# Optimization experiments

Measured on AMD Instinct MI355X. Metric: run time of the kernel, lower is better.

## Reference

```python
import jax, jax.numpy as jnp
import numpy as np

B, BANDS, N, IN_C, F, C = 4096, 5, 30, 512, 128, 9

def setup_inputs() -> dict:
    key = jax.random.key(0)
    ks = jax.random.split(key, 10)
    def glorot(k, shape):
        lim = float(np.sqrt(6.0 / (shape[0] + shape[-1])))
        return jax.random.uniform(k, shape, jnp.float32, -lim, lim)
    return {
        "real": jax.random.normal(ks[0], (B, N, IN_C), jnp.float32),
        "imag": jax.random.normal(ks[1], (B, N, IN_C), jnp.float32),
        "graph": jax.random.normal(ks[2], (B, BANDS, N, N), jnp.float32),
        "W1": glorot(ks[3], (IN_C, F)),
        "b1": jnp.zeros((F,), jnp.float32),
        "W2": glorot(ks[4], (F, F)),
        "b2": jnp.zeros((F,), jnp.float32),
        "Wlin": glorot(ks[5], (F, 1)),
        "blin": jnp.zeros((1,), jnp.float32),
        "Wconv": glorot(ks[6], (C, N)),  # Conv1d(30, C, k=1) weight squeezed
        "bconv": jnp.zeros((C,), jnp.float32),
    }

def _norm_adj(graph):
    # adj = mean over bands; PyG from_scipy_sparse_matrix keeps only the
    # nonzero PATTERN (edge weights are discarded in the original code).
    adj = jnp.mean(graph, axis=1)                       # [B, N, N]
    A = (adj != 0).astype(jnp.float32)
    eye = jnp.eye(A.shape[-1], dtype=jnp.float32)
    A_hat = jnp.where(eye > 0, 1.0, A)                  # add remaining self-loops
    deg = A_hat.sum(-1)                                 # [B, N]
    dinv = jnp.where(deg > 0, jax.lax.rsqrt(deg), 0.0)
    return dinv[..., :, None] * A_hat * dinv[..., None, :]  # D^-1/2 (A+I) D^-1/2

def reference(real, imag, graph, W1, b1, W2, b2, Wlin, blin, Wconv, bconv):
    An = _norm_adj(graph)                               # [B, N, N]
    # GCNConv layer 1: propagate(x @ W) + bias, then ReLU (dropout = eval identity)
    h = jnp.einsum('bnm,bmf->bnf', An, real @ W1) + b1
    h = jax.nn.relu(h)
    # GCNConv layer 2
    h = jnp.einsum('bnm,bmf->bnf', An, h @ W2) + b2
    h = jax.nn.relu(h)
    # lin: [B, N, F] -> [B, N], relu, then Conv1d(30->C, k=1) over length-1 axis
    x = jax.nn.relu((h @ Wlin + blin).squeeze(-1))      # [B, N]
    out = x @ Wconv.T + bconv                           # [B, C]
    return out
```

## Files before the change

### kernel.cpp

```cpp
#include <hip/hip_runtime.h>
#include <cstdint>

#define B_SZ 4096
#define NN   30
#define INC  512
#define FF   128
#define CC   9

typedef short short8 __attribute__((ext_vector_type(8)));
typedef float f32x4 __attribute__((ext_vector_type(4)));
typedef unsigned short us4 __attribute__((ext_vector_type(4)));

__device__ inline void split_bf16(float x, unsigned short& hi, unsigned short& lo) {
  uint32_t bits = __float_as_uint(x);
  hi = (unsigned short)(bits >> 16);
  float hif = __uint_as_float(((uint32_t)hi) << 16);
  float r = x - hif;
  lo = (unsigned short)(__float_as_uint(r) >> 16);
}

__global__ __launch_bounds__(128) void k_norm_adj(const float* __restrict__ graph,
                                                  float* __restrict__ An) {
  __shared__ float Ah[NN * NN];
  __shared__ float dinv[NN];
  const int b = blockIdx.x;
  const float* g = graph + (long)b * 5 * NN * NN;
  for (int e = threadIdx.x; e < NN * NN; e += 128) {
    float s = g[e] + g[e + 900] + g[e + 1800] + g[e + 2700] + g[e + 3600];
    float mean = s * 0.2f;
    int i = e / NN;
    int j = e - i * NN;
    Ah[e] = (mean != 0.0f || i == j) ? 1.0f : 0.0f;
  }
  __syncthreads();
  if (threadIdx.x < NN) {
    float d = 0.f;
#pragma unroll
    for (int j = 0; j < NN; ++j) d += Ah[threadIdx.x * NN + j];
    dinv[threadIdx.x] = (d > 0.f) ? (1.0f / sqrtf(d)) : 0.0f;
  }
  __syncthreads();
  float* ob = An + (long)b * NN * NN;
  for (int e = threadIdx.x; e < NN * NN; e += 128) {
    int i = e / NN;
    int j = e - i * NN;
    ob[e] = Ah[e] * dinv[i] * dinv[j];
  }
}

__global__ __launch_bounds__(256) void k_prep_w(const float* __restrict__ W,
                                                unsigned short* __restrict__ Wth,
                                                unsigned short* __restrict__ Wtl,
                                                int K) {
  int idx = blockIdx.x * 256 + threadIdx.x;
  if (idx >= K * FF) return;
  int k = idx >> 7;
  int n = idx & 127;
  unsigned short h, l;
  split_bf16(W[idx], h, l);
  Wth[n * K + k] = h;
  Wtl[n * K + k] = l;
}

#define LDT 40
#define LDY 132

__global__ __launch_bounds__(256, 2) void k_fused(
    const float* __restrict__ real,
    const float* __restrict__ An,
    const unsigned short* __restrict__ W1h, const unsigned short* __restrict__ W1l,
    const unsigned short* __restrict__ W2h, const unsigned short* __restrict__ W2l,
    const float* __restrict__ b1v, const float* __restrict__ b2v,
    const float* __restrict__ Wlin, const float* __restrict__ blin,
    const float* __restrict__ Wconv, const float* __restrict__ bconv,
    float* __restrict__ out) {
  __shared__ __align__(16) char smem[65168];
  unsigned short* H1h = (unsigned short*)smem;
  unsigned short* H1l = (unsigned short*)(smem + 16384);
  unsigned short* Ash = (unsigned short*)(smem + 32768);
  unsigned short* Asl = (unsigned short*)(smem + 32768 + 64 * LDT * 2);
  float* Ylds = (float*)(smem + 32768);
  float* partial = (float*)(smem + 64448);
  float* xs = (float*)(smem + 64928);

  const int tid = threadIdx.x;
  const int wave = tid >> 6;
  const int lane = tid & 63;
  const int fr = lane & 15;
  const int fq = lane >> 4;
  const int wc = wave;
  const long b0 = (long)blockIdx.x * 2;

  f32x4 acc[4][2];
#pragma unroll
  for (int i = 0; i < 4; ++i)
#pragma unroll
    for (int j = 0; j < 2; ++j) acc[i][j] = (f32x4){0.f, 0.f, 0.f, 0.f};

  const int r0 = tid >> 3, kq0 = tid & 7;
  const int r1 = r0 + 32;
  int i0 = r0 & 31; if (i0 >= NN) i0 -= NN;
  int i1 = r1 & 31; if (i1 >= NN) i1 -= NN;
  const float* aptr0 = real + ((b0 + (r0 >> 5)) * NN + i0) * (long)INC + kq0 * 4;
  const float* aptr1 = real + ((b0 + (r1 >> 5)) * NN + i1) * (long)INC + kq0 * 4;

  float4 pA0 = *(const float4*)(aptr0);
  float4 pA1 = *(const float4*)(aptr1);

  for (int k0 = 0; k0 < INC; k0 += 32) {
    __syncthreads();
    {
      us4 h, l;
      split_bf16(pA0.x, ((unsigned short*)&h)[0], ((unsigned short*)&l)[0]);
      split_bf16(pA0.y, ((unsigned short*)&h)[1], ((unsigned short*)&l)[1]);
      split_bf16(pA0.z, ((unsigned short*)&h)[2], ((unsigned short*)&l)[2]);
      split_bf16(pA0.w, ((unsigned short*)&h)[3], ((unsigned short*)&l)[3]);
      *(us4*)(Ash + r0 * LDT + kq0 * 4) = h;
      *(us4*)(Asl + r0 * LDT + kq0 * 4) = l;
      split_bf16(pA1.x, ((unsigned short*)&h)[0], ((unsigned short*)&l)[0]);
      split_bf16(pA1.y, ((unsigned short*)&h)[1], ((unsigned short*)&l)[1]);
      split_bf16(pA1.z, ((unsigned short*)&h)[2], ((unsigned short*)&l)[2]);
      split_bf16(pA1.w, ((unsigned short*)&h)[3], ((unsigned short*)&l)[3]);
      *(us4*)(Ash + r1 * LDT + kq0 * 4) = h;
      *(us4*)(Asl + r1 * LDT + kq0 * 4) = l;
    }
    if (k0 + 32 < INC) {
      pA0 = *(const float4*)(aptr0 + k0 + 32);
      pA1 = *(const float4*)(aptr1 + k0 + 32);
    }
    __syncthreads();
    short8 bh[2], bl2[2];
#pragma unroll
    for (int ct = 0; ct < 2; ++ct) {
      const long n = wc * 32 + ct * 16 + fr;
      bh[ct]  = *(const short8*)(W1h + n * INC + k0 + fq * 8);
      bl2[ct] = *(const short8*)(W1l + n * INC + k0 + fq * 8);
    }
#pragma unroll
    for (int rt = 0; rt < 4; ++rt) {
      const int m = rt * 16 + fr;
      short8 ah = *(const short8*)(Ash + m * LDT + fq * 8);
      short8 al = *(const short8*)(Asl + m * LDT + fq * 8);
#pragma unroll
      for (int ct = 0; ct < 2; ++ct) {
        acc[rt][ct] = __builtin_amdgcn_mfma_f32_16x16x32_bf16(ah, bh[ct], acc[rt][ct], 0, 0, 0);
        acc[rt][ct] = __builtin_amdgcn_mfma_f32_16x16x32_bf16(al, bh[ct], acc[rt][ct], 0, 0, 0);
        acc[rt][ct] = __builtin_amdgcn_mfma_f32_16x16x32_bf16(ah, bl2[ct], acc[rt][ct], 0, 0, 0);
      }
    }
  }
  __syncthreads();

#pragma unroll
  for (int rt = 0; rt < 4; ++rt) {
#pragma unroll
    for (int r = 0; r < 4; ++r) {
      const int row = rt * 16 + fq * 4 + r;
      const int ii = row & 31;
      if (ii < NN) {
        const int yrow = (row >> 5) * NN + ii;
#pragma unroll
        for (int ct = 0; ct < 2; ++ct)
          Ylds[yrow * LDY + wc * 32 + ct * 16 + fr] = acc[rt][ct][r];
      }
    }
  }
  {
    const int pr = wave;
    const int prow = (pr >> 1) * 32 + 30 + (pr & 1);
    *(uint32_t*)(H1h + prow * 128 + lane * 2) = 0u;
    *(uint32_t*)(H1l + prow * 128 + lane * 2) = 0u;
  }
  __syncthreads();

  const int f = tid & 127;
  const int bu = __builtin_amdgcn_readfirstlane(tid >> 7);
  const float* Arow = An + (b0 + bu) * (NN * NN);
  {
    float y[NN];
#pragma unroll
    for (int m = 0; m < NN; ++m) y[m] = Ylds[(bu * NN + m) * LDY + f];
    const float bias1 = b1v[f];
#pragma unroll 1
    for (int i = 0; i < NN; ++i) {
      float h = bias1;
#pragma unroll
      for (int m = 0; m < NN; ++m) h = fmaf(Arow[i * NN + m], y[m], h);
      h = fmaxf(h, 0.f);
      unsigned short hh, hl;
      split_bf16(h, hh, hl);
      const int row = bu * 32 + i;
      const int idx = row * 128 + ((((f >> 3) ^ (row & 7)) << 3) | (f & 7));
      H1h[idx] = hh;
      H1l[idx] = hl;
    }
  }
  __syncthreads();

  f32x4 acc2[4][2];
#pragma unroll
  for (int i = 0; i < 4; ++i)
#pragma unroll
    for (int j = 0; j < 2; ++j) acc2[i][j] = (f32x4){0.f, 0.f, 0.f, 0.f};

#pragma unroll
  for (int ks = 0; ks < 4; ++ks) {
    short8 bh[2], bl2[2];
#pragma unroll
    for (int ct = 0; ct < 2; ++ct) {
      const long n = wc * 32 + ct * 16 + fr;
      bh[ct]  = *(const short8*)(W2h + n * FF + ks * 32 + fq * 8);
      bl2[ct] = *(const short8*)(W2l + n * FF + ks * 32 + fq * 8);
    }
#pragma unroll
    for (int rt = 0; rt < 4; ++rt) {
      const int row = rt * 16 + fr;
      const int gs = (((ks * 4 + fq) ^ (row & 7)) << 3);
      short8 ah = *(const short8*)(H1h + row * 128 + gs);
      short8 al = *(const short8*)(H1l + row * 128 + gs);
#pragma unroll
      for (int ct = 0; ct < 2; ++ct) {
        acc2[rt][ct] = __builtin_amdgcn_mfma_f32_16x16x32_bf16(ah, bh[ct], acc2[rt][ct], 0, 0, 0);
        acc2[rt][ct] = __builtin_amdgcn_mfma_f32_16x16x32_bf16(al, bh[ct], acc2[rt][ct], 0, 0, 0);
        acc2[rt][ct] = __builtin_amdgcn_mfma_f32_16x16x32_bf16(ah, bl2[ct], acc2[rt][ct], 0, 0, 0);
      }
    }
  }
#pragma unroll
  for (int rt = 0; rt < 4; ++rt) {
#pragma unroll
    for (int r = 0; r < 4; ++r) {
      const int row = rt * 16 + fq * 4 + r;
      const int ii = row & 31;
      if (ii < NN) {
        const int yrow = (row >> 5) * NN + ii;
#pragma unroll
        for (int ct = 0; ct < 2; ++ct)
          Ylds[yrow * LDY + wc * 32 + ct * 16 + fr] = acc2[rt][ct][r];
      }
    }
  }
  __syncthreads();

  {
    float t[NN];
#pragma unroll
    for (int m = 0; m < NN; ++m) t[m] = Ylds[(bu * NN + m) * LDY + f];
    const float bias2 = b2v[f];
    const float wl = Wlin[f];
#pragma unroll 1
    for (int i = 0; i < NN; ++i) {
      float h = bias2;
#pragma unroll
      for (int m = 0; m < NN; ++m) h = fmaf(Arow[i * NN + m], t[m], h);
      float c = fmaxf(h, 0.f) * wl;
#pragma unroll
      for (int off = 32; off > 0; off >>= 1) c += __shfl_down(c, off, 64);
      if (lane == 0) partial[wave * NN + i] = c;
    }
  }
  __syncthreads();
  if (tid < 2 * NN) {
    const int bb = tid / NN, i = tid - bb * NN;
    float x = partial[bb * 2 * NN + i] + partial[(bb * 2 + 1) * NN + i] + blin[0];
    xs[bb * NN + i] = fmaxf(x, 0.f);
  }
  __syncthreads();
  if (tid < 2 * CC) {
    const int bb = tid / CC, c = tid - bb * CC;
    float o = bconv[c];
#pragma unroll
    for (int i = 0; i < NN; ++i) o = fmaf(xs[bb * NN + i], Wconv[c * NN + i], o);
    out[(b0 + bb) * CC + c] = o;
  }
}

extern "C" void kernel_launch(void* const* d_in, const int* in_sizes, int n_in,
                              void* d_out, int out_size, void* d_ws, size_t ws_size,
                              hipStream_t stream) {
  const float* real  = (const float*)d_in[0];
  const float* graph = (const float*)d_in[2];
  const float* W1    = (const float*)d_in[3];
  const float* b1    = (const float*)d_in[4];
  const float* W2    = (const float*)d_in[5];
  const float* b2    = (const float*)d_in[6];
  const float* Wlin  = (const float*)d_in[7];
  const float* blin  = (const float*)d_in[8];
  const float* Wconv = (const float*)d_in[9];
  const float* bconv = (const float*)d_in[10];
  float* out = (float*)d_out;

  float* An = (float*)d_ws;
  unsigned short* W1h = (unsigned short*)(An + (long)B_SZ * NN * NN);
  unsigned short* W1l = W1h + INC * FF;
  unsigned short* W2h = W1l + INC * FF;
  unsigned short* W2l = W2h + FF * FF;

  k_norm_adj<<<B_SZ, 128, 0, stream>>>(graph, An);
  k_prep_w<<<(INC * FF + 255) / 256, 256, 0, stream>>>(W1, W1h, W1l, INC);
  k_prep_w<<<(FF * FF + 255) / 256, 256, 0, stream>>>(W2, W2h, W2l, FF);
  k_fused<<<B_SZ / 2, 256, 0, stream>>>(real, An, W1h, W1l, W2h, W2l,
                                        b1, b2, Wlin, blin, Wconv, bconv, out);
}
```

Before: 651.7 us.

## Fuse adjacency normalization into main kernel, one batch per block, double-buffer staging

```diff
diff --git a/kernel.cpp b/kernel.cpp
--- a/kernel.cpp
+++ b/kernel.cpp
@@ -19,33 +19,33 @@
   lo = (unsigned short)(__float_as_uint(r) >> 16);
 }
 
-__global__ __launch_bounds__(128) void k_norm_adj(const float* __restrict__ graph,
-                                                  float* __restrict__ An) {
-  __shared__ float Ah[NN * NN];
-  __shared__ float dinv[NN];
-  const int b = blockIdx.x;
-  const float* g = graph + (long)b * 5 * NN * NN;
-  for (int e = threadIdx.x; e < NN * NN; e += 128) {
-    float s = g[e] + g[e + 900] + g[e + 1800] + g[e + 2700] + g[e + 3600];
-    float mean = s * 0.2f;
-    int i = e / NN;
-    int j = e - i * NN;
-    Ah[e] = (mean != 0.0f || i == j) ? 1.0f : 0.0f;
-  }
-  __syncthreads();
-  if (threadIdx.x < NN) {
-    float d = 0.f;
-#pragma unroll
-    for (int j = 0; j < NN; ++j) d += Ah[threadIdx.x * NN + j];
-    dinv[threadIdx.x] = (d > 0.f) ? (1.0f / sqrtf(d)) : 0.0f;
-  }
-  __syncthreads();
-  float* ob = An + (long)b * NN * NN;
-  for (int e = threadIdx.x; e < NN * NN; e += 128) {
-    int i = e / NN;
-    int j = e - i * NN;
-    ob[e] = Ah[e] * dinv[i] * dinv[j];
-  }
+__device__ inline void split4(const float4 v, us4& h, us4& l) {
+  unsigned short* hp = (unsigned short*)&h;
+  unsigned short* lp = (unsigned short*)&l;
+  split_bf16(v.x, hp[0], lp[0]);
+  split_bf16(v.y, hp[1], lp[1]);
+  split_bf16(v.z, hp[2], lp[2]);
+  split_bf16(v.w, hp[3], lp[3]);
+}
+
+__device__ inline void split8(const float4 v0, const float4 v1, short8& h, short8& l) {
+  unsigned short* hp = (unsigned short*)&h;
+  unsigned short* lp = (unsigned short*)&l;
+  split_bf16(v0.x, hp[0], lp[0]);
+  split_bf16(v0.y, hp[1], lp[1]);
+  split_bf16(v0.z, hp[2], lp[2]);
+  split_bf16(v0.w, hp[3], lp[3]);
+  split_bf16(v1.x, hp[4], lp[4]);
+  split_bf16(v1.y, hp[5], lp[5]);
+  split_bf16(v1.z, hp[6], lp[6]);
+  split_bf16(v1.w, hp[7], lp[7]);
+}
+
+__device__ inline void wg_barrier() {
+  __builtin_amdgcn_sched_barrier(0);
+  asm volatile("s_waitcnt lgkmcnt(0)" ::: "memory");
+  __builtin_amdgcn_s_barrier();
+  __builtin_amdgcn_sched_barrier(0);
 }
 
 __global__ __launch_bounds__(256) void k_prep_w(const float* __restrict__ W,
@@ -64,214 +64,282 @@
 
 #define LDT 40
 #define LDY 132
-
-__global__ __launch_bounds__(256, 2) void k_fused(
+#define ANW 32
+
+__global__ __launch_bounds__(256, 4) void k_fused(
     const float* __restrict__ real,
-    const float* __restrict__ An,
+    const float* __restrict__ graph,
     const unsigned short* __restrict__ W1h, const unsigned short* __restrict__ W1l,
     const unsigned short* __restrict__ W2h, const unsigned short* __restrict__ W2l,
     const float* __restrict__ b1v, const float* __restrict__ b2v,
     const float* __restrict__ Wlin, const float* __restrict__ blin,
     const float* __restrict__ Wconv, const float* __restrict__ bconv,
     float* __restrict__ out) {
-  __shared__ __align__(16) char smem[65168];
-  unsigned short* H1h = (unsigned short*)smem;
-  unsigned short* H1l = (unsigned short*)(smem + 16384);
-  unsigned short* Ash = (unsigned short*)(smem + 32768);
-  unsigned short* Asl = (unsigned short*)(smem + 32768 + 64 * LDT * 2);
-  float* Ylds = (float*)(smem + 32768);
-  float* partial = (float*)(smem + 64448);
-  float* xs = (float*)(smem + 64928);
+  __shared__ __align__(16) float AnL[NN * ANW];
+  __shared__ float dinvL[NN + 2];
+  __shared__ __align__(16) char stageY[15840];
+  __shared__ __align__(16) float H1[32 * LDY];
+  __shared__ float partial[2][NN];
+  __shared__ float xs[NN];
+
+  unsigned short* Sh = (unsigned short*)stageY;
+  unsigned short* Sl = (unsigned short*)(stageY + 2 * 32 * LDT * 2);
+  float* Ylds = (float*)stageY;
 
   const int tid = threadIdx.x;
   const int wave = tid >> 6;
   const int lane = tid & 63;
   const int fr = lane & 15;
   const int fq = lane >> 4;
-  const int wc = wave;
-  const long b0 = (long)blockIdx.x * 2;
-
-  f32x4 acc[4][2];
-#pragma unroll
-  for (int i = 0; i < 4; ++i)
+  const int wc = wave * 32;
+  const long b = blockIdx.x;
+
+  float4 g0, g1, g2, g3, g4;
+  const int e4 = tid * 4;
+  const bool gact = (e4 < NN * NN);
+  {
+    const float* gp = graph + b * 5 * NN * NN + (gact ? e4 : 0);
+    g0 = *(const float4*)(gp);
+    g1 = *(const float4*)(gp + 900);
+    g2 = *(const float4*)(gp + 1800);
+    g3 = *(const float4*)(gp + 2700);
+    g4 = *(const float4*)(gp + 3600);
+  }
+
+  const int arow = tid >> 3;
+  const int akq = tid & 7;
+  const int ar = arow < NN ? arow : NN - 1;
+  const float* abase = real + (b * NN + ar) * (long)INC + akq * 4;
+  float4 pa[2];
+  pa[0] = *(const float4*)(abase);
+  pa[1] = *(const float4*)(abase + 32);
+
+  const unsigned short* w1hp = W1h + (long)(wc + fr) * INC + fq * 8;
+  const unsigned short* w1lp = W1l + (long)(wc + fr) * INC + fq * 8;
+  short8 bh0 = *(const short8*)(w1hp);
+  short8 bh1 = *(const short8*)(w1hp + 16 * INC);
+  short8 bl0 = *(const short8*)(w1lp);
+  short8 bl1 = *(const short8*)(w1lp + 16 * INC);
+
+  if (gact) {
+    float mm0 = g0.x + g1.x + g2.x + g3.x + g4.x;
+    float mm1 = g0.y + g1.y + g2.y + g3.y + g4.y;
+    float mm2 = g0.z + g1.z + g2.z + g3.z + g4.z;
+    float mm3 = g0.w + g1.w + g2.w + g3.w + g4.w;
+    float mm[4] = {mm0, mm1, mm2, mm3};
+#pragma unroll
+    for (int q = 0; q < 4; ++q) {
+      int e = e4 + q;
+      int i = e / NN, j = e - i * NN;
+      AnL[i * ANW + j] = (mm[q] * 0.2f != 0.0f || i == j) ? 1.0f : 0.0f;
+    }
+  }
+  if (tid < NN) { AnL[tid * ANW + 30] = 0.f; AnL[tid * ANW + 31] = 0.f; }
+  wg_barrier();
+  if (tid < NN) {
+    float d = 0.f;
+    const float4* r4 = (const float4*)(AnL + tid * ANW);
+#pragma unroll
+    for (int q = 0; q < 8; ++q) { float4 v = r4[q]; d += v.x + v.y + v.z + v.w; }
+    dinvL[tid] = (d > 0.f) ? (1.0f / sqrtf(d)) : 0.f;
+  }
+  wg_barrier();
+  if (gact) {
+#pragma unroll
+    for (int q = 0; q < 4; ++q) {
+      int e = e4 + q;
+      int i = e / NN, j = e - i * NN;
+      AnL[i * ANW + j] *= dinvL[i] * dinvL[j];
+    }
+  }
+
+  {
+    us4 h, l;
+    split4(pa[0], h, l);
+    *(us4*)(Sh + arow * LDT + akq * 4) = h;
+    *(us4*)(Sl + arow * LDT + akq * 4) = l;
+  }
+  pa[0] = *(const float4*)(abase + 64);
+  wg_barrier();
+
+  f32x4 acc[2][2];
+#pragma unroll
+  for (int i = 0; i < 2; ++i)
 #pragma unroll
     for (int j = 0; j < 2; ++j) acc[i][j] = (f32x4){0.f, 0.f, 0.f, 0.f};
 
-  const int r0 = tid >> 3, kq0 = tid & 7;
-  const int r1 = r0 + 32;
-  int i0 = r0 & 31; if (i0 >= NN) i0 -= NN;
-  int i1 = r1 & 31; if (i1 >= NN) i1 -= NN;
-  const float* aptr0 = real + ((b0 + (r0 >> 5)) * NN + i0) * (long)INC + kq0 * 4;
-  const float* aptr1 = real + ((b0 + (r1 >> 5)) * NN + i1) * (long)INC + kq0 * 4;
-
-  float4 pA0 = *(const float4*)(aptr0);
-  float4 pA1 = *(const float4*)(aptr1);
-
-  for (int k0 = 0; k0 < INC; k0 += 32) {
-    __syncthreads();
-    {
+#pragma unroll
+  for (int t = 0; t < 16; ++t) {
+    const int cur = t & 1;
+    const int nxt = cur ^ 1;
+    short8 ah0 = *(const short8*)(Sh + cur * 32 * LDT + fr * LDT + fq * 8);
+    short8 ah1 = *(const short8*)(Sh + cur * 32 * LDT + (16 + fr) * LDT + fq * 8);
+    short8 al0 = *(const short8*)(Sl + cur * 32 * LDT + fr * LDT + fq * 8);
+    short8 al1 = *(const short8*)(Sl + cur * 32 * LDT + (16 + fr) * LDT + fq * 8);
+
+    short8 nbh0, nbh1, nbl0, nbl1;
+    if (t + 1 < 16) {
       us4 h, l;
-      split_bf16(pA0.x, ((unsigned short*)&h)[0], ((unsigned short*)&l)[0]);
-      split_bf16(pA0.y, ((unsigned short*)&h)[1], ((unsigned short*)&l)[1]);
-      split_bf16(pA0.z, ((unsigned short*)&h)[2], ((unsigned short*)&l)[2]);
-      split_bf16(pA0.w, ((unsigned short*)&h)[3], ((unsigned short*)&l)[3]);
-      *(us4*)(Ash + r0 * LDT + kq0 * 4) = h;
-      *(us4*)(Asl + r0 * LDT + kq0 * 4) = l;
-      split_bf16(pA1.x, ((unsigned short*)&h)[0], ((unsigned short*)&l)[0]);
-      split_bf16(pA1.y, ((unsigned short*)&h)[1], ((unsigned short*)&l)[1]);
-      split_bf16(pA1.z, ((unsigned short*)&h)[2], ((unsigned short*)&l)[2]);
-      split_bf16(pA1.w, ((unsigned short*)&h)[3], ((unsigned short*)&l)[3]);
-      *(us4*)(Ash + r1 * LDT + kq0 * 4) = h;
-      *(us4*)(Asl + r1 * LDT + kq0 * 4) = l;
-    }
-    if (k0 + 32 < INC) {
-      pA0 = *(const float4*)(aptr0 + k0 + 32);
-      pA1 = *(const float4*)(aptr1 + k0 + 32);
-    }
-    __syncthreads();
-    short8 bh[2], bl2[2];
-#pragma unroll
-    for (int ct = 0; ct < 2; ++ct) {
-      const long n = wc * 32 + ct * 16 + fr;
-      bh[ct]  = *(const short8*)(W1h + n * INC + k0 + fq * 8);
-      bl2[ct] = *(const short8*)(W1l + n * INC + k0 + fq * 8);
-    }
-#pragma unroll
-    for (int rt = 0; rt < 4; ++rt) {
-      const int m = rt * 16 + fr;
-      short8 ah = *(const short8*)(Ash + m * LDT + fq * 8);
-      short8 al = *(const short8*)(Asl + m * LDT + fq * 8);
-#pragma unroll
-      for (int ct = 0; ct < 2; ++ct) {
-        acc[rt][ct] = __builtin_amdgcn_mfma_f32_16x16x32_bf16(ah, bh[ct], acc[rt][ct], 0, 0, 0);
-        acc[rt][ct] = __builtin_amdgcn_mfma_f32_16x16x32_bf16(al, bh[ct], acc[rt][ct], 0, 0, 0);
-        acc[rt][ct] = __builtin_amdgcn_mfma_f32_16x16x32_bf16(ah, bl2[ct], acc[rt][ct], 0, 0, 0);
-      }
-    }
-  }
-  __syncthreads();
-
-#pragma unroll
-  for (int rt = 0; rt < 4; ++rt) {
+      split4(pa[(t + 1) & 1], h, l);
+      *(us4*)(Sh + nxt * 32 * LDT + arow * LDT + akq * 4) = h;
+      *(us4*)(Sl + nxt * 32 * LDT + arow * LDT + akq * 4) = l;
+      if (t + 3 < 16) pa[(t + 1) & 1] = *(const float4*)(abase + (t + 3) * 32);
+      nbh0 = *(const short8*)(w1hp + (t + 1) * 32);
+      nbh1 = *(const short8*)(w1hp + 16 * INC + (t + 1) * 32);
+      nbl0 = *(const short8*)(w1lp + (t + 1) * 32);
+      nbl1 = *(const short8*)(w1lp + 16 * INC + (t + 1) * 32);
+    }
+
+    acc[0][0] = __builtin_amdgcn_mfma_f32_16x16x32_bf16(ah0, bh0, acc[0][0], 0, 0, 0);
+    acc[0][0] = __builtin_amdgcn_mfma_f32_16x16x32_bf16(al0, bh0, acc[0][0], 0, 0, 0);
+    acc[0][0] = __builtin_amdgcn_mfma_f32_16x16x32_bf16(ah0, bl0, acc[0][0], 0, 0, 0);
+    acc[0][1] = __builtin_amdgcn_mfma_f32_16x16x32_bf16(ah0, bh1, acc[0][1], 0, 0, 0);
+    acc[0][1] = __builtin_amdgcn_mfma_f32_16x16x32_bf16(al0, bh1, acc[0][1], 0, 0, 0);
+    acc[0][1] = __builtin_amdgcn_mfma_f32_16x16x32_bf16(ah0, bl1, acc[0][1], 0, 0, 0);
+    acc[1][0] = __builtin_amdgcn_mfma_f32_16x16x32_bf16(ah1, bh0, acc[1][0], 0, 0, 0);
+    acc[1][0] = __builtin_amdgcn_mfma_f32_16x16x32_bf16(al1, bh0, acc[1][0], 0, 0, 0);
+    acc[1][0] = __builtin_amdgcn_mfma_f32_16x16x32_bf16(ah1, bl0, acc[1][0], 0, 0, 0);
+    acc[1][1] = __builtin_amdgcn_mfma_f32_16x16x32_bf16(ah1, bh1, acc[1][1], 0, 0, 0);
+    acc[1][1] = __builtin_amdgcn_mfma_f32_16x16x32_bf16(al1, bh1, acc[1][1], 0, 0, 0);
+    acc[1][1] = __builtin_amdgcn_mfma_f32_16x16x32_bf16(ah1, bl1, acc[1][1], 0, 0, 0);
+
+    wg_barrier();
+    if (t + 1 < 16) { bh0 = nbh0; bh1 = nbh1; bl0 = nbl0; bl1 = nbl1; }
+  }
+
+#pragma unroll
+  for (int rt = 0; rt < 2; ++rt)
 #pragma unroll
     for (int r = 0; r < 4; ++r) {
       const int row = rt * 16 + fq * 4 + r;
-      const int ii = row & 31;
-      if (ii < NN) {
-        const int yrow = (row >> 5) * NN + ii;
+      if (row < NN) {
 #pragma unroll
         for (int ct = 0; ct < 2; ++ct)
-          Ylds[yrow * LDY + wc * 32 + ct * 16 + fr] = acc[rt][ct][r];
+          Ylds[row * LDY + wc + ct * 16 + fr] = acc[rt][ct][r];
       }
     }
-  }
+  wg_barrier();
+
+  const int f = tid & 127;
+  const int half = tid >> 7;
+  const int i0 = half * 15;
+  const float bias1 = b1v[f];
+
+  const unsigned short* w2hp = W2h + (long)(wc + fr) * FF + fq * 8;
+  const unsigned short* w2lp = W2l + (long)(wc + fr) * FF + fq * 8;
+  short8 c2h0 = *(const short8*)(w2hp);
+  short8 c2h1 = *(const short8*)(w2hp + 16 * FF);
+  short8 c2l0 = *(const short8*)(w2lp);
+  short8 c2l1 = *(const short8*)(w2lp + 16 * FF);
+
   {
-    const int pr = wave;
-    const int prow = (pr >> 1) * 32 + 30 + (pr & 1);
-    *(uint32_t*)(H1h + prow * 128 + lane * 2) = 0u;
-    *(uint32_t*)(H1l + prow * 128 + lane * 2) = 0u;
-  }
-  __syncthreads();
-
-  const int f = tid & 127;
-  const int bu = __builtin_amdgcn_readfirstlane(tid >> 7);
-  const float* Arow = An + (b0 + bu) * (NN * NN);
-  {
-    float y[NN];
-#pragma unroll
-    for (int m = 0; m < NN; ++m) y[m] = Ylds[(bu * NN + m) * LDY + f];
-    const float bias1 = b1v[f];
+    float y[NN + 2];
+#pragma unroll
+    for (int m = 0; m < NN; ++m) y[m] = Ylds[m * LDY + f];
+    y[30] = 0.f; y[31] = 0.f;
 #pragma unroll 1
-    for (int i = 0; i < NN; ++i) {
-      float h = bias1;
-#pragma unroll
-      for (int m = 0; m < NN; ++m) h = fmaf(Arow[i * NN + m], y[m], h);
-      h = fmaxf(h, 0.f);
-      unsigned short hh, hl;
-      split_bf16(h, hh, hl);
-      const int row = bu * 32 + i;
-      const int idx = row * 128 + ((((f >> 3) ^ (row & 7)) << 3) | (f & 7));
-      H1h[idx] = hh;
-      H1l[idx] = hl;
-    }
-  }
-  __syncthreads();
-
-  f32x4 acc2[4][2];
-#pragma unroll
-  for (int i = 0; i < 4; ++i)
+    for (int i = i0; i < i0 + 15; ++i) {
+      const float4* a4 = (const float4*)(AnL + i * ANW);
+      float s0 = 0.f, s1 = 0.f;
+#pragma unroll
+      for (int q = 0; q < 8; ++q) {
+        float4 v = a4[q];
+        s0 = fmaf(v.x, y[4 * q + 0], s0);
+        s1 = fmaf(v.y, y[4 * q + 1], s1);
+        s0 = fmaf(v.z, y[4 * q + 2], s0);
+        s1 = fmaf(v.w, y[4 * q + 3], s1);
+      }
+      H1[i * LDY + f] = fmaxf(s0 + s1 + bias1, 0.f);
+    }
+  }
+  wg_barrier();
+
+  f32x4 acc2[2][2];
+#pragma unroll
+  for (int i = 0; i < 2; ++i)
 #pragma unroll
     for (int j = 0; j < 2; ++j) acc2[i][j] = (f32x4){0.f, 0.f, 0.f, 0.f};
 
 #pragma unroll
   for (int ks = 0; ks < 4; ++ks) {
-    short8 bh[2], bl2[2];
-#pragma unroll
-    for (int ct = 0; ct < 2; ++ct) {
-      const long n = wc * 32 + ct * 16 + fr;
-      bh[ct]  = *(const short8*)(W2h + n * FF + ks * 32 + fq * 8);
-      bl2[ct] = *(const short8*)(W2l + n * FF + ks * 32 + fq * 8);
-    }
-#pragma unroll
-    for (int rt = 0; rt < 4; ++rt) {
-      const int row = rt * 16 + fr;
-      const int gs = (((ks * 4 + fq) ^ (row & 7)) << 3);
-      short8 ah = *(const short8*)(H1h + row * 128 + gs);
-      short8 al = *(const short8*)(H1l + row * 128 + gs);
-#pragma unroll
-      for (int ct = 0; ct < 2; ++ct) {
-        acc2[rt][ct] = __builtin_amdgcn_mfma_f32_16x16x32_bf16(ah, bh[ct], acc2[rt][ct], 0, 0, 0);
-        acc2[rt][ct] = __builtin_amdgcn_mfma_f32_16x16x32_bf16(al, bh[ct], acc2[rt][ct], 0, 0, 0);
-        acc2[rt][ct] = __builtin_amdgcn_mfma_f32_16x16x32_bf16(ah, bl2[ct], acc2[rt][ct], 0, 0, 0);
-      }
-    }
-  }
-#pragma unroll
-  for (int rt = 0; rt < 4; ++rt) {
+    short8 a2h0, a2h1, a2l0, a2l1;
+    {
+      const float* hp0 = H1 + fr * LDY + ks * 32 + fq * 8;
+      const float* hp1 = H1 + (16 + fr) * LDY + ks * 32 + fq * 8;
+      split8(*(const float4*)(hp0), *(const float4*)(hp0 + 4), a2h0, a2l0);
+      split8(*(const float4*)(hp1), *(const float4*)(hp1 + 4), a2h1, a2l1);
+    }
+    short8 n2h0, n2h1, n2l0, n2l1;
+    if (ks + 1 < 4) {
+      n2h0 = *(const short8*)(w2hp + (ks + 1) * 32);
+      n2h1 = *(const short8*)(w2hp + 16 * FF + (ks + 1) * 32);
+      n2l0 = *(const short8*)(w2lp + (ks + 1) * 32);
+      n2l1 = *(const short8*)(w2lp + 16 * FF + (ks + 1) * 32);
+    }
+    acc2[0][0] = __builtin_amdgcn_mfma_f32_16x16x32_bf16(a2h0, c2h0, acc2[0][0], 0, 0, 0);
+    acc2[0][0] = __builtin_amdgcn_mfma_f32_16x16x32_bf16(a2l0, c2h0, acc2[0][0], 0, 0, 0);
+    acc2[0][0] = __builtin_amdgcn_mfma_f32_16x16x32_bf16(a2h0, c2l0, acc2[0][0], 0, 0, 0);
+    acc2[0][1] = __builtin_amdgcn_mfma_f32_16x16x32_bf16(a2h0, c2h1, acc2[0][1], 0, 0, 0);
+    acc2[0][1] = __builtin_amdgcn_mfma_f32_16x16x32_bf16(a2l0, c2h1, acc2[0][1], 0, 0, 0);
+    acc2[0][1] = __builtin_amdgcn_mfma_f32_16x16x32_bf16(a2h0, c2l1, acc2[0][1], 0, 0, 0);
+    acc2[1][0] = __builtin_amdgcn_mfma_f32_16x16x32_bf16(a2h1, c2h0, acc2[1][0], 0, 0, 0);
+    acc2[1][0] = __builtin_amdgcn_mfma_f32_16x16x32_bf16(a2l1, c2h0, acc2[1][0], 0, 0, 0);
+    acc2[1][0] = __builtin_amdgcn_mfma_f32_16x16x32_bf16(a2h1, c2l0, acc2[1][0], 0, 0, 0);
+    acc2[1][1] = __builtin_amdgcn_mfma_f32_16x16x32_bf16(a2h1, c2h1, acc2[1][1], 0, 0, 0);
+    acc2[1][1] = __builtin_amdgcn_mfma_f32_16x16x32_bf16(a2l1, c2h1, acc2[1][1], 0, 0, 0);
+    acc2[1][1] = __builtin_amdgcn_mfma_f32_16x16x32_bf16(a2h1, c2l1, acc2[1][1], 0, 0, 0);
+    if (ks + 1 < 4) { c2h0 = n2h0; c2h1 = n2h1; c2l0 = n2l0; c2l1 = n2l1; }
+  }
+
+#pragma unroll
+  for (int rt = 0; rt < 2; ++rt)
 #pragma unroll
     for (int r = 0; r < 4; ++r) {
       const int row = rt * 16 + fq * 4 + r;
-      const int ii = row & 31;
-      if (ii < NN) {
-        const int yrow = (row >> 5) * NN + ii;
+      if (row < NN) {
 #pragma unroll
         for (int ct = 0; ct < 2; ++ct)
-          Ylds[yrow * LDY + wc * 32 + ct * 16 + fr] = acc2[rt][ct][r];
+          Ylds[row * LDY + wc + ct * 16 + fr] = acc2[rt][ct][r];
       }
     }
-  }
-  __syncthreads();
+  wg_barrier();
 
   {
-    float t[NN];
-#pragma unroll
-    for (int m = 0; m < NN; ++m) t[m] = Ylds[(bu * NN + m) * LDY + f];
     const float bias2 = b2v[f];
     const float wl = Wlin[f];
+    float tr[NN + 2];
+#pragma unroll
+    for (int m = 0; m < NN; ++m) tr[m] = Ylds[m * LDY + f];
+    tr[30] = 0.f; tr[31] = 0.f;
 #pragma unroll 1
-    for (int i = 0; i < NN; ++i) {
-      float h = bias2;
-#pragma unroll
-      for (int m = 0; m < NN; ++m) h = fmaf(Arow[i * NN + m], t[m], h);
-      float c = fmaxf(h, 0.f) * wl;
+    for (int i = i0; i < i0 + 15; ++i) {
+      const float4* a4 = (const float4*)(AnL + i * ANW);
+      float s0 = 0.f, s1 = 0.f;
+#pragma unroll
+      for (int q = 0; q < 8; ++q) {
+        float4 v = a4[q];
+        s0 = fmaf(v.x, tr[4 * q + 0], s0);
+        s1 = fmaf(v.y, tr[4 * q + 1], s1);
+        s0 = fmaf(v.z, tr[4 * q + 2], s0);
+        s1 = fmaf(v.w, tr[4 * q + 3], s1);
+      }
+      float c = fmaxf(s0 + s1 + bias2, 0.f) * wl;
 #pragma unroll
       for (int off = 32; off > 0; off >>= 1) c += __shfl_down(c, off, 64);
-      if (lane == 0) partial[wave * NN + i] = c;
-    }
-  }
-  __syncthreads();
-  if (tid < 2 * NN) {
-    const int bb = tid / NN, i = tid - bb * NN;
-    float x = partial[bb * 2 * NN + i] + partial[(bb * 2 + 1) * NN + i] + blin[0];
-    xs[bb * NN + i] = fmaxf(x, 0.f);
-  }
-  __syncthreads();
-  if (tid < 2 * CC) {
-    const int bb = tid / CC, c = tid - bb * CC;
-    float o = bconv[c];
-#pragma unroll
-    for (int i = 0; i < NN; ++i) o = fmaf(xs[bb * NN + i], Wconv[c * NN + i], o);
-    out[(b0 + bb) * CC + c] = o;
+      if (lane == 0) partial[(tid >> 6) & 1][i] = c;
+    }
+  }
+  wg_barrier();
+  if (tid < NN) {
+    float x = partial[0][tid] + partial[1][tid] + blin[0];
+    xs[tid] = fmaxf(x, 0.f);
+  }
+  wg_barrier();
+  if (tid < CC) {
+    float o = bconv[tid];
+#pragma unroll
+    for (int i = 0; i < NN; ++i) o = fmaf(xs[i], Wconv[tid * NN + i], o);
+    out[b * CC + tid] = o;
   }
 }
 
@@ -290,15 +358,13 @@
   const float* bconv = (const float*)d_in[10];
   float* out = (float*)d_out;
 
-  float* An = (float*)d_ws;
-  unsigned short* W1h = (unsigned short*)(An + (long)B_SZ * NN * NN);
+  unsigned short* W1h = (unsigned short*)d_ws;
   unsigned short* W1l = W1h + INC * FF;
   unsigned short* W2h = W1l + INC * FF;
   unsigned short* W2l = W2h + FF * FF;
 
-  k_norm_adj<<<B_SZ, 128, 0, stream>>>(graph, An);
   k_prep_w<<<(INC * FF + 255) / 256, 256, 0, stream>>>(W1, W1h, W1l, INC);
   k_prep_w<<<(FF * FF + 255) / 256, 256, 0, stream>>>(W2, W2h, W2l, FF);
-  k_fused<<<B_SZ / 2, 256, 0, stream>>>(real, An, W1h, W1l, W2h, W2l,
-                                        b1, b2, Wlin, blin, Wconv, bconv, out);
-}
+  k_fused<<<B_SZ, 256, 0, stream>>>(real, graph, W1h, W1l, W2h, W2l,
+                                    b1, b2, Wlin, blin, Wconv, bconv, out);
+}
```

Result: faster. 613.9 us (-5.8%).
